# Kernel tuning notes

Hardware: AMD Instinct MI355X
Metric: run time of the kernel (lower is better)

The kernel has to match this reference:

```python
import jax, jax.numpy as jnp
import numpy as np

N_NODES = 100000
N_EDGES = 500000
D = 128          # node embedding dim; in_channels = 2*D = 256
HID = 256
OUT = 1


def setup_inputs() -> dict:
    key = jax.random.key(0)
    k1, k2, k3, k4, k5 = jax.random.split(key, 5)
    z = jax.random.normal(k1, (N_NODES, D), dtype=jnp.float32)
    z2 = jax.random.normal(k2, (N_NODES, D), dtype=jnp.float32)
    edge = jax.random.randint(k3, (2, N_EDGES), 0, N_NODES, dtype=jnp.int64)
    # MLP params (Linear stored as [in, out] for x @ W + b)
    W1 = jax.random.normal(k4, (2 * D, HID), dtype=jnp.float32) * (1.0 / np.sqrt(2 * D))
    b1 = jnp.zeros((HID,), dtype=jnp.float32)
    W2 = jax.random.normal(k5, (HID, OUT), dtype=jnp.float32) * (1.0 / np.sqrt(HID))
    b2 = jnp.zeros((OUT,), dtype=jnp.float32)
    return {"z": z, "z2": z2, "edge": edge, "W1": W1, "b1": b1, "W2": W2, "b2": b2}


def reference(z, z2, edge, W1, b1, W2, b2):
    # Gather node embeddings at edge endpoints, elementwise multiply, concat.
    src, dst = edge[0], edge[1]
    x = jnp.concatenate([z[src] * z[dst], z2[src] * z2[dst]], axis=1)  # [E, 2D]
    # Two-layer MLP (dropout is identity in eval mode), relu, final sigmoid.
    h = jax.nn.relu(x @ W1 + b1)        # [E, HID]
    out = jax.nn.sigmoid(h @ W2 + b2)   # [E, 1]
    return out
```

## Files before the change

### kernel.cpp

```cpp
#include <hip/hip_runtime.h>
#include <hip/hip_bf16.h>
#include <math.h>

typedef _Float16 half8 __attribute__((ext_vector_type(8)));
typedef float f32x4 __attribute__((ext_vector_type(4)));

#define NE 500000
#define ND 128
#define NNODES 100000
#define NT ((NE + 63) / 64)
#define TPB 8

__global__ void prep_w1t_kernel(const float* __restrict__ W1,
                                _Float16* __restrict__ W1T) {
    int i = blockIdx.x * blockDim.x + threadIdx.x;
    int n = i >> 8, k = i & 255;
    W1T[n * 256 + k] = (_Float16)W1[k * 256 + n];
}

__global__ __launch_bounds__(256) void prep_zh_kernel(
    const float* __restrict__ z, const float* __restrict__ z2,
    _Float16* __restrict__ zh, _Float16* __restrict__ z2h) {
    long t = (long)blockIdx.x * 256 + threadIdx.x;
    const float* src; _Float16* dst; long off;
    const long halfn = (long)NNODES * ND / 8;
    if (t < halfn) { src = z;  dst = zh;  off = t * 8; }
    else           { src = z2; dst = z2h; off = (t - halfn) * 8; }
    float4 a = *reinterpret_cast<const float4*>(src + off);
    float4 b = *reinterpret_cast<const float4*>(src + off + 4);
    half8 v;
    v[0] = (_Float16)a.x; v[1] = (_Float16)a.y;
    v[2] = (_Float16)a.z; v[3] = (_Float16)a.w;
    v[4] = (_Float16)b.x; v[5] = (_Float16)b.y;
    v[6] = (_Float16)b.z; v[7] = (_Float16)b.w;
    *reinterpret_cast<half8*>(dst + off) = v;
}

#define PUBLISH_BARRIER() do { \
    asm volatile("s_waitcnt lgkmcnt(0)" ::: "memory"); \
    __builtin_amdgcn_s_barrier(); } while (0)

__global__ __launch_bounds__(512, 1) void edge_mlp_pipe(
    const _Float16* __restrict__ zh, const _Float16* __restrict__ z2h,
    const int* __restrict__ edge,
    const _Float16* __restrict__ w1t,
    const float* __restrict__ b1, const float* __restrict__ W2,
    const float* __restrict__ b2, float* __restrict__ out)
{
    __shared__ _Float16 xs[64 * 256];
    __shared__ float partials[4][64];

    const int tid = threadIdx.x;
    const int lane = tid & 63;
    const int wv = tid >> 6;
    const int mi = wv >> 2;
    const int ni = wv & 3;
    const int l15 = lane & 15;
    const int l4 = lane >> 4;
    const int l5 = lane >> 5;
    const int hz = (lane >> 4) & 1;
    const int c8 = lane & 15;
    const _Float16* gbase = hz ? z2h : zh;

    half8 breg[4][8];
#pragma unroll
    for (int nf = 0; nf < 4; ++nf)
#pragma unroll
        for (int ks = 0; ks < 8; ++ks)
            breg[nf][ks] = *reinterpret_cast<const half8*>(
                w1t + (long)(ni * 64 + nf * 16 + l15) * 256 + ks * 32 + l4 * 8);

    float b1v[4], w2v[4];
#pragma unroll
    for (int nf = 0; nf < 4; ++nf) {
        int col = ni * 64 + nf * 16 + l15;
        b1v[nf] = b1[col];
        w2v[nf] = W2[col];
    }
    const float bias2 = b2[0];

    const int t0 = blockIdx.x * TPB;
    const int tend = (t0 + TPB < NT) ? (t0 + TPB) : NT;

    half8 vs[4], vd[4];
    int idx_nxt;

    {
        long e = (long)t0 * 64 + wv * 8 + (lane & 7); if (e >= NE) e = NE - 1;
        int myidx = edge[((lane >> 3) & 1) ? (NE + e) : e];
#pragma unroll
        for (int i = 0; i < 4; ++i) {
            int el_loc = i * 2 + l5;
            long s = __shfl(myidx, el_loc, 64);
            long d = __shfl(myidx, 8 + el_loc, 64);
            vs[i] = *reinterpret_cast<const half8*>(gbase + s * ND + (c8 << 3));
            vd[i] = *reinterpret_cast<const half8*>(gbase + d * ND + (c8 << 3));
        }
        int t1 = (t0 + 1 < NT) ? t0 + 1 : NT - 1;
        long e1 = (long)t1 * 64 + wv * 8 + (lane & 7); if (e1 >= NE) e1 = NE - 1;
        idx_nxt = edge[((lane >> 3) & 1) ? (NE + e1) : e1];
    }

    for (int t = t0; t < tend; ++t) {
#pragma unroll
        for (int i = 0; i < 4; ++i) {
            int el = wv * 8 + i * 2 + l5;
            half8 p = vs[i] * vd[i];
            int col0 = (hz << 7) + (c8 << 3);
            *reinterpret_cast<half8*>(&xs[el * 256 + (col0 ^ ((el & 7) << 3))]) = p;
        }

        if (t + 1 < tend) {
#pragma unroll
            for (int i = 0; i < 4; ++i) {
                int el_loc = i * 2 + l5;
                long s = __shfl(idx_nxt, el_loc, 64);
                long d = __shfl(idx_nxt, 8 + el_loc, 64);
                vs[i] = *reinterpret_cast<const half8*>(gbase + s * ND + (c8 << 3));
                vd[i] = *reinterpret_cast<const half8*>(gbase + d * ND + (c8 << 3));
            }
            int t2 = (t + 2 < NT) ? t + 2 : NT - 1;
            long e2 = (long)t2 * 64 + wv * 8 + (lane & 7); if (e2 >= NE) e2 = NE - 1;
            idx_nxt = edge[((lane >> 3) & 1) ? (NE + e2) : e2];
        }

        PUBLISH_BARRIER();

        f32x4 acc[2][4];
#pragma unroll
        for (int mf = 0; mf < 2; ++mf)
#pragma unroll
            for (int nf = 0; nf < 4; ++nf)
                acc[mf][nf] = (f32x4){0.f, 0.f, 0.f, 0.f};

#pragma unroll
        for (int ks = 0; ks < 8; ++ks) {
            const int k0 = ks * 32 + l4 * 8;
            half8 a[2];
#pragma unroll
            for (int mf = 0; mf < 2; ++mf) {
                int row = mi * 32 + mf * 16 + l15;
                a[mf] = *reinterpret_cast<const half8*>(
                    &xs[row * 256 + (k0 ^ ((row & 7) << 3))]);
            }
#pragma unroll
            for (int mf = 0; mf < 2; ++mf)
#pragma unroll
                for (int nf = 0; nf < 4; ++nf)
                    acc[mf][nf] = __builtin_amdgcn_mfma_f32_16x16x32_f16(
                        a[mf], breg[nf][ks], acc[mf][nf], 0, 0, 0);
        }

#pragma unroll
        for (int mf = 0; mf < 2; ++mf) {
            float s0 = 0.f, s1 = 0.f, s2 = 0.f, s3 = 0.f;
#pragma unroll
            for (int nf = 0; nf < 4; ++nf) {
                float h0 = fmaxf(acc[mf][nf][0] + b1v[nf], 0.f);
                float h1 = fmaxf(acc[mf][nf][1] + b1v[nf], 0.f);
                float h2 = fmaxf(acc[mf][nf][2] + b1v[nf], 0.f);
                float h3 = fmaxf(acc[mf][nf][3] + b1v[nf], 0.f);
                s0 += h0 * w2v[nf]; s1 += h1 * w2v[nf];
                s2 += h2 * w2v[nf]; s3 += h3 * w2v[nf];
            }
#pragma unroll
            for (int mask = 1; mask < 16; mask <<= 1) {
                s0 += __shfl_xor(s0, mask, 64);
                s1 += __shfl_xor(s1, mask, 64);
                s2 += __shfl_xor(s2, mask, 64);
                s3 += __shfl_xor(s3, mask, 64);
            }
            if (l15 == 0) {
                int rb = mi * 32 + mf * 16 + l4 * 4;
                partials[ni][rb + 0] = s0;
                partials[ni][rb + 1] = s1;
                partials[ni][rb + 2] = s2;
                partials[ni][rb + 3] = s3;
            }
        }
        PUBLISH_BARRIER();

        if (tid < 64) {
            float p = partials[0][tid] + partials[1][tid]
                    + partials[2][tid] + partials[3][tid] + bias2;
            long e = (long)t * 64 + tid;
            if (e < NE) out[e] = 1.0f / (1.0f + expf(-p));
        }
    }
}

__global__ __launch_bounds__(256) void edge_mlp_f32(
    const float* __restrict__ z, const float* __restrict__ z2,
    const int* __restrict__ edge,
    const _Float16* __restrict__ w1t,
    const float* __restrict__ b1, const float* __restrict__ W2,
    const float* __restrict__ b2, float* __restrict__ out)
{
    __shared__ _Float16 xs[64 * 256];
    __shared__ float partials[4][64];
    const int tid = threadIdx.x, lane = tid & 63, wv = tid >> 6;
    const int l15 = lane & 15, l4 = lane >> 4;
    const long eb0 = (long)blockIdx.x * 64;
    {
        const int hz = lane >> 5, c4 = lane & 31;
        const float* base = hz ? z2 : z;
        for (int i = 0; i < 16; ++i) {
            int el = (wv << 4) + i;
            long ee = eb0 + el; if (ee >= NE) ee = NE - 1;
            long s = edge[ee], d = edge[NE + ee];
            float4 a = *reinterpret_cast<const float4*>(base + s * ND + (c4 << 2));
            float4 b = *reinterpret_cast<const float4*>(base + d * ND + (c4 << 2));
            _Float16 p[4] = {(_Float16)(a.x * b.x), (_Float16)(a.y * b.y),
                             (_Float16)(a.z * b.z), (_Float16)(a.w * b.w)};
            int col0 = (hz << 7) + (c4 << 2);
            int o = el * 256 + (col0 ^ ((el & 7) << 3));
            xs[o] = p[0]; xs[o + 1] = p[1]; xs[o + 2] = p[2]; xs[o + 3] = p[3];
        }
    }
    __syncthreads();
    f32x4 acc[4][4];
    for (int m = 0; m < 4; ++m) for (int n = 0; n < 4; ++n) acc[m][n] = (f32x4){0,0,0,0};
    const int ncol0 = wv * 64 + l15;
    for (int ks = 0; ks < 8; ++ks) {
        const int k0 = ks * 32 + l4 * 8;
        half8 a[4], b[4];
        for (int m = 0; m < 4; ++m) {
            int row = m * 16 + l15;
            a[m] = *reinterpret_cast<const half8*>(&xs[row * 256 + (k0 ^ ((row & 7) << 3))]);
        }
        for (int n = 0; n < 4; ++n)
            b[n] = *reinterpret_cast<const half8*>(w1t + (long)(ncol0 + n * 16) * 256 + k0);
        for (int m = 0; m < 4; ++m) for (int n = 0; n < 4; ++n)
            acc[m][n] = __builtin_amdgcn_mfma_f32_16x16x32_f16(a[m], b[n], acc[m][n], 0, 0, 0);
    }
    float b1v[4], w2v[4];
    for (int n = 0; n < 4; ++n) {
        int col = wv * 64 + n * 16 + l15;
        b1v[n] = b1[col]; w2v[n] = W2[col];
    }
    for (int m = 0; m < 4; ++m) {
        float s0 = 0, s1 = 0, s2 = 0, s3 = 0;
        for (int n = 0; n < 4; ++n) {
            float h0 = fmaxf(acc[m][n][0] + b1v[n], 0.f), h1 = fmaxf(acc[m][n][1] + b1v[n], 0.f);
            float h2 = fmaxf(acc[m][n][2] + b1v[n], 0.f), h3 = fmaxf(acc[m][n][3] + b1v[n], 0.f);
            s0 += h0 * w2v[n]; s1 += h1 * w2v[n]; s2 += h2 * w2v[n]; s3 += h3 * w2v[n];
        }
        for (int mask = 1; mask < 16; mask <<= 1) {
            s0 += __shfl_xor(s0, mask, 64); s1 += __shfl_xor(s1, mask, 64);
            s2 += __shfl_xor(s2, mask, 64); s3 += __shfl_xor(s3, mask, 64);
        }
        if (l15 == 0) {
            int rb = m * 16 + l4 * 4;
            partials[wv][rb] = s0; partials[wv][rb + 1] = s1;
            partials[wv][rb + 2] = s2; partials[wv][rb + 3] = s3;
        }
    }
    __syncthreads();
    if (tid < 64) {
        float p = partials[0][tid] + partials[1][tid] + partials[2][tid]
                + partials[3][tid] + b2[0];
        long e = eb0 + tid;
        if (e < NE) out[e] = 1.0f / (1.0f + expf(-p));
    }
}

extern "C" void kernel_launch(void* const* d_in, const int* in_sizes, int n_in,
                              void* d_out, int out_size, void* d_ws, size_t ws_size,
                              hipStream_t stream)
{
    const float* z  = (const float*)d_in[0];
    const float* z2 = (const float*)d_in[1];
    const int*  edge = (const int*)d_in[2];
    const float* W1 = (const float*)d_in[3];
    const float* b1 = (const float*)d_in[4];
    const float* W2 = (const float*)d_in[5];
    const float* b2 = (const float*)d_in[6];
    float* out = (float*)d_out;

    const size_t zh_bytes = (size_t)NNODES * ND * 2;
    const size_t need = 2 * zh_bytes + 256 * 256 * 2;
    const bool mirrors = (ws_size >= need);

    _Float16* zh  = (_Float16*)d_ws;
    _Float16* z2h = (_Float16*)((char*)d_ws + zh_bytes);
    _Float16* w1t = mirrors
        ? (_Float16*)((char*)d_ws + 2 * zh_bytes)
        : (_Float16*)d_ws;

    prep_w1t_kernel<<<256, 256, 0, stream>>>(W1, w1t);
    if (mirrors) {
        prep_zh_kernel<<<12500, 256, 0, stream>>>(z, z2, zh, z2h);
        const int nblk = (NT + TPB - 1) / TPB;
        edge_mlp_pipe<<<nblk, 512, 0, stream>>>(
            zh, z2h, edge, w1t, b1, W2, b2, out);
    } else {
        edge_mlp_f32<<<NT, 256, 0, stream>>>(
            z, z2, edge, w1t, b1, W2, b2, out);
    }
}
```

Measured before the change: 154.4 us.

## Gather endpoint rows into double-buffered LDS via async global_load_lds

Replaces the register-staged gather (load to VGPRs, multiply, store to LDS) with direct global-to-LDS async loads of raw source and destination rows into double-buffered shared arrays. The elementwise product moves into the MFMA operand load, and the output write is spread across all waves. The aim is to drop the VGPR round-trip and overlap the next tile's gather with the current GEMM using a vmcnt-based wait. It doubles the LDS footprint and relies on the swizzle and vmcnt(10) count being right, and the product is now recomputed for each of the two mf fragments.

```diff
diff --git a/kernel.cpp b/kernel.cpp
--- a/kernel.cpp
+++ b/kernel.cpp
@@ -36,18 +36,15 @@
     *reinterpret_cast<half8*>(dst + off) = v;
 }
 
-#define PUBLISH_BARRIER() do { \
-    asm volatile("s_waitcnt lgkmcnt(0)" ::: "memory"); \
-    __builtin_amdgcn_s_barrier(); } while (0)
-
-__global__ __launch_bounds__(512, 1) void edge_mlp_pipe(
+__global__ __launch_bounds__(512, 1) void edge_mlp_dma(
     const _Float16* __restrict__ zh, const _Float16* __restrict__ z2h,
     const int* __restrict__ edge,
     const _Float16* __restrict__ w1t,
     const float* __restrict__ b1, const float* __restrict__ W2,
     const float* __restrict__ b2, float* __restrict__ out)
 {
-    __shared__ _Float16 xs[64 * 256];
+    __shared__ _Float16 rawS[2][64][256];
+    __shared__ _Float16 rawD[2][64][256];
     __shared__ float partials[4][64];
 
     const int tid = threadIdx.x;
@@ -57,10 +54,45 @@
     const int ni = wv & 3;
     const int l15 = lane & 15;
     const int l4 = lane >> 4;
-    const int l5 = lane >> 5;
-    const int hz = (lane >> 4) & 1;
-    const int c8 = lane & 15;
-    const _Float16* gbase = hz ? z2h : zh;
+
+    const int dl5 = lane >> 5;
+    const int dcc = lane & 15;
+    const int dten = (lane >> 4) & 1;
+    const _Float16* dbase = dten ? z2h : zh;
+
+    const int t0 = blockIdx.x * TPB;
+    const int tend = (t0 + TPB < NT) ? (t0 + TPB) : NT;
+
+#define LOAD_IDX(TT, DST) do {                                               \
+        int tt_ = (TT) < (NT - 1) ? (TT) : (NT - 1);                         \
+        long e_ = (long)tt_ * 64 + wv * 8 + (lane & 7);                      \
+        if (e_ >= NE) e_ = NE - 1;                                           \
+        (DST) = edge[(((lane >> 3) & 1) ? (long)NE : 0L) + e_];              \
+    } while (0)
+
+#define ISSUE_DMA(IDXREG, BB) do {                                           \
+        _Pragma("unroll")                                                    \
+        for (int j = 0; j < 4; ++j) {                                        \
+            int sl_ = 2 * j + dl5;                                           \
+            int si_ = __shfl((IDXREG), sl_, 64);                             \
+            int di_ = __shfl((IDXREG), 8 + sl_, 64);                         \
+            int swz_ = (dcc ^ sl_) << 3;  \
+            const _Float16* gs_ = dbase + (long)si_ * ND + swz_;             \
+            const _Float16* gd_ = dbase + (long)di_ * ND + swz_;             \
+            __builtin_amdgcn_global_load_lds(                                \
+                (const void*)gs_, (void*)&rawS[BB][wv * 8 + 2 * j][0], 16, 0, 0); \
+            __builtin_amdgcn_global_load_lds(                                \
+                (const void*)gd_, (void*)&rawD[BB][wv * 8 + 2 * j][0], 16, 0, 0); \
+        }                                                                    \
+    } while (0)
+
+    int idx_cur, idx_new;
+    {
+        int idx0;
+        LOAD_IDX(t0, idx0);
+        ISSUE_DMA(idx0, 0);
+        LOAD_IDX(t0 + 1, idx_cur);
+    }
 
     half8 breg[4][8];
 #pragma unroll
@@ -79,52 +111,15 @@
     }
     const float bias2 = b2[0];
 
-    const int t0 = blockIdx.x * TPB;
-    const int tend = (t0 + TPB < NT) ? (t0 + TPB) : NT;
-
-    half8 vs[4], vd[4];
-    int idx_nxt;
-
-    {
-        long e = (long)t0 * 64 + wv * 8 + (lane & 7); if (e >= NE) e = NE - 1;
-        int myidx = edge[((lane >> 3) & 1) ? (NE + e) : e];
-#pragma unroll
-        for (int i = 0; i < 4; ++i) {
-            int el_loc = i * 2 + l5;
-            long s = __shfl(myidx, el_loc, 64);
-            long d = __shfl(myidx, 8 + el_loc, 64);
-            vs[i] = *reinterpret_cast<const half8*>(gbase + s * ND + (c8 << 3));
-            vd[i] = *reinterpret_cast<const half8*>(gbase + d * ND + (c8 << 3));
-        }
-        int t1 = (t0 + 1 < NT) ? t0 + 1 : NT - 1;
-        long e1 = (long)t1 * 64 + wv * 8 + (lane & 7); if (e1 >= NE) e1 = NE - 1;
-        idx_nxt = edge[((lane >> 3) & 1) ? (NE + e1) : e1];
-    }
-
     for (int t = t0; t < tend; ++t) {
-#pragma unroll
-        for (int i = 0; i < 4; ++i) {
-            int el = wv * 8 + i * 2 + l5;
-            half8 p = vs[i] * vd[i];
-            int col0 = (hz << 7) + (c8 << 3);
-            *reinterpret_cast<half8*>(&xs[el * 256 + (col0 ^ ((el & 7) << 3))]) = p;
-        }
-
-        if (t + 1 < tend) {
-#pragma unroll
-            for (int i = 0; i < 4; ++i) {
-                int el_loc = i * 2 + l5;
-                long s = __shfl(idx_nxt, el_loc, 64);
-                long d = __shfl(idx_nxt, 8 + el_loc, 64);
-                vs[i] = *reinterpret_cast<const half8*>(gbase + s * ND + (c8 << 3));
-                vd[i] = *reinterpret_cast<const half8*>(gbase + d * ND + (c8 << 3));
-            }
-            int t2 = (t + 2 < NT) ? t + 2 : NT - 1;
-            long e2 = (long)t2 * 64 + wv * 8 + (lane & 7); if (e2 >= NE) e2 = NE - 1;
-            idx_nxt = edge[((lane >> 3) & 1) ? (NE + e2) : e2];
-        }
-
-        PUBLISH_BARRIER();
+        const int cur = (t - t0) & 1, nxt = cur ^ 1;
+
+        ISSUE_DMA(idx_cur, nxt);
+        LOAD_IDX(t + 2, idx_new);
+
+        asm volatile("s_waitcnt vmcnt(10)" ::: "memory");
+        __builtin_amdgcn_s_barrier();
+        __builtin_amdgcn_sched_barrier(0);
 
         f32x4 acc[2][4];
 #pragma unroll
@@ -133,22 +128,25 @@
             for (int nf = 0; nf < 4; ++nf)
                 acc[mf][nf] = (f32x4){0.f, 0.f, 0.f, 0.f};
 
+        const _Float16* rs = &rawS[cur][0][0];
+        const _Float16* rd = &rawD[cur][0][0];
 #pragma unroll
         for (int ks = 0; ks < 8; ++ks) {
-            const int k0 = ks * 32 + l4 * 8;
-            half8 a[2];
+            const int c = ks * 4 + l4;
+            const int slot = ((c & 15) ^ (l15 & 7)) | (c & 16);
+            const int so = slot * 8;
 #pragma unroll
             for (int mf = 0; mf < 2; ++mf) {
                 int row = mi * 32 + mf * 16 + l15;
-                a[mf] = *reinterpret_cast<const half8*>(
-                    &xs[row * 256 + (k0 ^ ((row & 7) << 3))]);
-            }
-#pragma unroll
-            for (int mf = 0; mf < 2; ++mf)
+                int o = row * 256 + so;
+                half8 aS = *reinterpret_cast<const half8*>(rs + o);
+                half8 aD = *reinterpret_cast<const half8*>(rd + o);
+                half8 a = aS * aD;
 #pragma unroll
                 for (int nf = 0; nf < 4; ++nf)
                     acc[mf][nf] = __builtin_amdgcn_mfma_f32_16x16x32_f16(
-                        a[mf], breg[nf][ks], acc[mf][nf], 0, 0, 0);
+                        a, breg[nf][ks], acc[mf][nf], 0, 0, 0);
+            }
         }
 
 #pragma unroll
@@ -178,15 +176,21 @@
                 partials[ni][rb + 3] = s3;
             }
         }
-        PUBLISH_BARRIER();
-
-        if (tid < 64) {
-            float p = partials[0][tid] + partials[1][tid]
-                    + partials[2][tid] + partials[3][tid] + bias2;
-            long e = (long)t * 64 + tid;
+        asm volatile("s_waitcnt lgkmcnt(0)" ::: "memory");
+        __builtin_amdgcn_s_barrier();
+        __builtin_amdgcn_sched_barrier(0);
+
+        if (lane < 8) {
+            int r = wv * 8 + lane;
+            float p = partials[0][r] + partials[1][r]
+                    + partials[2][r] + partials[3][r] + bias2;
+            long e = (long)t * 64 + r;
             if (e < NE) out[e] = 1.0f / (1.0f + expf(-p));
         }
-    }
+        idx_cur = idx_new;
+    }
+#undef LOAD_IDX
+#undef ISSUE_DMA
 }
 
 __global__ __launch_bounds__(256) void edge_mlp_f32(
@@ -291,7 +295,7 @@
     if (mirrors) {
         prep_zh_kernel<<<12500, 256, 0, stream>>>(z, z2, zh, z2h);
         const int nblk = (NT + TPB - 1) / TPB;
-        edge_mlp_pipe<<<nblk, 512, 0, stream>>>(
+        edge_mlp_dma<<<nblk, 512, 0, stream>>>(
             zh, z2h, edge, w1t, b1, W2, b2, out);
     } else {
         edge_mlp_f32<<<NT, 256, 0, stream>>>(
```

New measurement: 178.9 us. +15.9%, slower.

## Interleave z/z2 fp16 mirror rows and stage W1 in LDS via async copy

Applied to the files above, without the earlier changes.

Packs z and z2 into one interleaved fp16 row per node so each edge endpoint becomes a single contiguous 512-byte gather, using readlane broadcast indices with half4 per-lane loads. W1 is pre-swizzled and copied into LDS with global_load_lds instead of being held as 32 half8 registers per lane, freeing VGPRs at the cost of 128KB LDS and extra LDS reads per MFMA step. Adds extra barriers per tile and reuses the xs buffer for partial sums. The output writes are spread across waves.

```diff
diff --git a/kernel.cpp b/kernel.cpp
--- a/kernel.cpp
+++ b/kernel.cpp
@@ -2,6 +2,7 @@
 #include <hip/hip_bf16.h>
 #include <math.h>
 
+typedef _Float16 half4 __attribute__((ext_vector_type(4)));
 typedef _Float16 half8 __attribute__((ext_vector_type(8)));
 typedef float f32x4 __attribute__((ext_vector_type(4)));
 
@@ -11,44 +12,48 @@
 #define NT ((NE + 63) / 64)
 #define TPB 8
 
-__global__ void prep_w1t_kernel(const float* __restrict__ W1,
-                                _Float16* __restrict__ W1T) {
-    int i = blockIdx.x * blockDim.x + threadIdx.x;
-    int n = i >> 8, k = i & 255;
-    W1T[n * 256 + k] = (_Float16)W1[k * 256 + n];
-}
-
-__global__ __launch_bounds__(256) void prep_zh_kernel(
+__global__ __launch_bounds__(256) void prep_zi_kernel(
     const float* __restrict__ z, const float* __restrict__ z2,
-    _Float16* __restrict__ zh, _Float16* __restrict__ z2h) {
+    _Float16* __restrict__ zi) {
     long t = (long)blockIdx.x * 256 + threadIdx.x;
-    const float* src; _Float16* dst; long off;
-    const long halfn = (long)NNODES * ND / 8;
-    if (t < halfn) { src = z;  dst = zh;  off = t * 8; }
-    else           { src = z2; dst = z2h; off = (t - halfn) * 8; }
-    float4 a = *reinterpret_cast<const float4*>(src + off);
-    float4 b = *reinterpret_cast<const float4*>(src + off + 4);
+    long idx = t * 8;
+    if (idx >= (long)NNODES * 256) return;
+    int node = (int)(idx >> 8), col = (int)(idx & 255);
+    const float* src = (col < 128) ? (z + (long)node * 128 + col)
+                                   : (z2 + (long)node * 128 + (col - 128));
+    float4 a = *reinterpret_cast<const float4*>(src);
+    float4 b = *reinterpret_cast<const float4*>(src + 4);
     half8 v;
     v[0] = (_Float16)a.x; v[1] = (_Float16)a.y;
     v[2] = (_Float16)a.z; v[3] = (_Float16)a.w;
     v[4] = (_Float16)b.x; v[5] = (_Float16)b.y;
     v[6] = (_Float16)b.z; v[7] = (_Float16)b.w;
-    *reinterpret_cast<half8*>(dst + off) = v;
+    *reinterpret_cast<half8*>(zi + idx) = v;
+}
+
+__global__ void prep_w1s_kernel(const float* __restrict__ W1,
+                                _Float16* __restrict__ w1s) {
+    int i = blockIdx.x * blockDim.x + threadIdx.x;
+    int col = i >> 8, k = i & 255;
+    int kk = (((k >> 3) ^ (col & 7)) << 3) | (k & 7);
+    w1s[col * 256 + kk] = (_Float16)W1[(long)k * 256 + col];
 }
 
 #define PUBLISH_BARRIER() do { \
     asm volatile("s_waitcnt lgkmcnt(0)" ::: "memory"); \
-    __builtin_amdgcn_s_barrier(); } while (0)
-
-__global__ __launch_bounds__(512, 1) void edge_mlp_pipe(
-    const _Float16* __restrict__ zh, const _Float16* __restrict__ z2h,
+    __builtin_amdgcn_s_barrier(); \
+    __builtin_amdgcn_sched_barrier(0); } while (0)
+
+__global__ __launch_bounds__(512, 1) void edge_mlp_v8(
+    const _Float16* __restrict__ zi,
     const int* __restrict__ edge,
-    const _Float16* __restrict__ w1t,
+    const _Float16* __restrict__ w1s,
     const float* __restrict__ b1, const float* __restrict__ W2,
     const float* __restrict__ b2, float* __restrict__ out)
 {
+    __shared__ _Float16 w1lds[256 * 256];
     __shared__ _Float16 xs[64 * 256];
-    __shared__ float partials[4][64];
+    float* ps = (float*)xs;
 
     const int tid = threadIdx.x;
     const int lane = tid & 63;
@@ -57,18 +62,15 @@
     const int ni = wv & 3;
     const int l15 = lane & 15;
     const int l4 = lane >> 4;
-    const int l5 = lane >> 5;
-    const int hz = (lane >> 4) & 1;
-    const int c8 = lane & 15;
-    const _Float16* gbase = hz ? z2h : zh;
-
-    half8 breg[4][8];
-#pragma unroll
-    for (int nf = 0; nf < 4; ++nf)
-#pragma unroll
-        for (int ks = 0; ks < 8; ++ks)
-            breg[nf][ks] = *reinterpret_cast<const half8*>(
-                w1t + (long)(ni * 64 + nf * 16 + l15) * 256 + ks * 32 + l4 * 8);
+
+    {
+        const char* gsrc = (const char*)w1s + (long)(wv * 16) * 1024 + lane * 16;
+        char* ldst = (char*)w1lds + (wv * 16) * 1024;
+#pragma unroll
+        for (int i = 0; i < 16; ++i)
+            __builtin_amdgcn_global_load_lds(
+                (const void*)(gsrc + i * 1024), (void*)(ldst + i * 1024), 16, 0, 0);
+    }
 
     float b1v[4], w2v[4];
 #pragma unroll
@@ -82,48 +84,42 @@
     const int t0 = blockIdx.x * TPB;
     const int tend = (t0 + TPB < NT) ? (t0 + TPB) : NT;
 
-    half8 vs[4], vd[4];
-    int idx_nxt;
-
-    {
-        long e = (long)t0 * 64 + wv * 8 + (lane & 7); if (e >= NE) e = NE - 1;
-        int myidx = edge[((lane >> 3) & 1) ? (NE + e) : e];
-#pragma unroll
-        for (int i = 0; i < 4; ++i) {
-            int el_loc = i * 2 + l5;
-            long s = __shfl(myidx, el_loc, 64);
-            long d = __shfl(myidx, 8 + el_loc, 64);
-            vs[i] = *reinterpret_cast<const half8*>(gbase + s * ND + (c8 << 3));
-            vd[i] = *reinterpret_cast<const half8*>(gbase + d * ND + (c8 << 3));
-        }
-        int t1 = (t0 + 1 < NT) ? t0 + 1 : NT - 1;
-        long e1 = (long)t1 * 64 + wv * 8 + (lane & 7); if (e1 >= NE) e1 = NE - 1;
-        idx_nxt = edge[((lane >> 3) & 1) ? (NE + e1) : e1];
-    }
+    half4 vs[8], vd[8];
+    int idx_cur, idx_nxt;
+
+#define LOAD_IDX(TT, DST) do {                                               \
+        long tt_ = (TT); if (tt_ > NT - 1) tt_ = NT - 1;                     \
+        long e_ = tt_ * 64 + wv * 8 + (lane & 7);                            \
+        if (e_ >= NE) e_ = NE - 1;                                           \
+        (DST) = edge[(((lane >> 3) & 1) ? (long)NE : 0L) + e_];              \
+    } while (0)
+
+#define ISSUE_GATHER(IDXREG) do {                                            \
+        _Pragma("unroll")                                                    \
+        for (int j = 0; j < 8; ++j) {                                        \
+            int s_ = __builtin_amdgcn_readlane((IDXREG), j);                 \
+            int d_ = __builtin_amdgcn_readlane((IDXREG), 8 + j);             \
+            vs[j] = *reinterpret_cast<const half4*>(zi + (long)s_ * 256 + lane * 4); \
+            vd[j] = *reinterpret_cast<const half4*>(zi + (long)d_ * 256 + lane * 4); \
+        }                                                                    \
+    } while (0)
+
+    LOAD_IDX(t0, idx_cur);
+    ISSUE_GATHER(idx_cur);
+    LOAD_IDX(t0 + 1, idx_cur);
 
     for (int t = t0; t < tend; ++t) {
 #pragma unroll
-        for (int i = 0; i < 4; ++i) {
-            int el = wv * 8 + i * 2 + l5;
-            half8 p = vs[i] * vd[i];
-            int col0 = (hz << 7) + (c8 << 3);
-            *reinterpret_cast<half8*>(&xs[el * 256 + (col0 ^ ((el & 7) << 3))]) = p;
-        }
-
+        for (int j = 0; j < 8; ++j) {
+            int e = wv * 8 + j;
+            half4 p = vs[j] * vd[j];
+            int boff = e * 512 + ((lane * 8) ^ ((e & 7) << 4));
+            *reinterpret_cast<half4*>((char*)xs + boff) = p;
+        }
         if (t + 1 < tend) {
-#pragma unroll
-            for (int i = 0; i < 4; ++i) {
-                int el_loc = i * 2 + l5;
-                long s = __shfl(idx_nxt, el_loc, 64);
-                long d = __shfl(idx_nxt, 8 + el_loc, 64);
-                vs[i] = *reinterpret_cast<const half8*>(gbase + s * ND + (c8 << 3));
-                vd[i] = *reinterpret_cast<const half8*>(gbase + d * ND + (c8 << 3));
-            }
-            int t2 = (t + 2 < NT) ? t + 2 : NT - 1;
-            long e2 = (long)t2 * 64 + wv * 8 + (lane & 7); if (e2 >= NE) e2 = NE - 1;
-            idx_nxt = edge[((lane >> 3) & 1) ? (NE + e2) : e2];
-        }
-
+            ISSUE_GATHER(idx_cur);
+            LOAD_IDX(t + 2, idx_nxt);
+        }
         PUBLISH_BARRIER();
 
         f32x4 acc[2][4];
@@ -135,21 +131,28 @@
 
 #pragma unroll
         for (int ks = 0; ks < 8; ++ks) {
-            const int k0 = ks * 32 + l4 * 8;
-            half8 a[2];
+            const int kb = ks * 64 + l4 * 16;
+            half8 a[2], bfr[4];
 #pragma unroll
             for (int mf = 0; mf < 2; ++mf) {
-                int row = mi * 32 + mf * 16 + l15;
+                int r = mi * 32 + mf * 16 + l15;
                 a[mf] = *reinterpret_cast<const half8*>(
-                    &xs[row * 256 + (k0 ^ ((row & 7) << 3))]);
+                    (const char*)xs + r * 512 + (kb ^ ((r & 7) << 4)));
+            }
+#pragma unroll
+            for (int nf = 0; nf < 4; ++nf) {
+                int c = ni * 64 + nf * 16 + l15;
+                bfr[nf] = *reinterpret_cast<const half8*>(
+                    (const char*)w1lds + c * 512 + (kb ^ ((c & 7) << 4)));
             }
 #pragma unroll
             for (int mf = 0; mf < 2; ++mf)
 #pragma unroll
                 for (int nf = 0; nf < 4; ++nf)
                     acc[mf][nf] = __builtin_amdgcn_mfma_f32_16x16x32_f16(
-                        a[mf], breg[nf][ks], acc[mf][nf], 0, 0, 0);
-        }
+                        a[mf], bfr[nf], acc[mf][nf], 0, 0, 0);
+        }
+        PUBLISH_BARRIER();
 
 #pragma unroll
         for (int mf = 0; mf < 2; ++mf) {
@@ -172,27 +175,31 @@
             }
             if (l15 == 0) {
                 int rb = mi * 32 + mf * 16 + l4 * 4;
-                partials[ni][rb + 0] = s0;
-                partials[ni][rb + 1] = s1;
-                partials[ni][rb + 2] = s2;
-                partials[ni][rb + 3] = s3;
+                ps[ni * 64 + rb + 0] = s0;
+                ps[ni * 64 + rb + 1] = s1;
+                ps[ni * 64 + rb + 2] = s2;
+                ps[ni * 64 + rb + 3] = s3;
             }
         }
         PUBLISH_BARRIER();
 
-        if (tid < 64) {
-            float p = partials[0][tid] + partials[1][tid]
-                    + partials[2][tid] + partials[3][tid] + bias2;
-            long e = (long)t * 64 + tid;
+        if (lane < 8) {
+            int r = wv * 8 + lane;
+            float p = ps[r] + ps[64 + r] + ps[128 + r] + ps[192 + r] + bias2;
+            long e = (long)t * 64 + r;
             if (e < NE) out[e] = 1.0f / (1.0f + expf(-p));
         }
-    }
+        idx_cur = idx_nxt;
+        PUBLISH_BARRIER();
+    }
+#undef LOAD_IDX
+#undef ISSUE_GATHER
 }
 
 __global__ __launch_bounds__(256) void edge_mlp_f32(
     const float* __restrict__ z, const float* __restrict__ z2,
     const int* __restrict__ edge,
-    const _Float16* __restrict__ w1t,
+    const _Float16* __restrict__ w1s,
     const float* __restrict__ b1, const float* __restrict__ W2,
     const float* __restrict__ b2, float* __restrict__ out)
 {
@@ -210,26 +217,27 @@
             long s = edge[ee], d = edge[NE + ee];
             float4 a = *reinterpret_cast<const float4*>(base + s * ND + (c4 << 2));
             float4 b = *reinterpret_cast<const float4*>(base + d * ND + (c4 << 2));
-            _Float16 p[4] = {(_Float16)(a.x * b.x), (_Float16)(a.y * b.y),
-                             (_Float16)(a.z * b.z), (_Float16)(a.w * b.w)};
             int col0 = (hz << 7) + (c4 << 2);
-            int o = el * 256 + (col0 ^ ((el & 7) << 3));
-            xs[o] = p[0]; xs[o + 1] = p[1]; xs[o + 2] = p[2]; xs[o + 3] = p[3];
+            int boff = el * 512 + (((col0 * 2) & ~15) ^ ((el & 7) << 4)) + ((col0 * 2) & 15);
+            _Float16* q = (_Float16*)((char*)xs + boff);
+            q[0] = (_Float16)(a.x * b.x); q[1] = (_Float16)(a.y * b.y);
+            q[2] = (_Float16)(a.z * b.z); q[3] = (_Float16)(a.w * b.w);
         }
     }
     __syncthreads();
     f32x4 acc[4][4];
     for (int m = 0; m < 4; ++m) for (int n = 0; n < 4; ++n) acc[m][n] = (f32x4){0,0,0,0};
-    const int ncol0 = wv * 64 + l15;
     for (int ks = 0; ks < 8; ++ks) {
-        const int k0 = ks * 32 + l4 * 8;
+        const int kb = ks * 64 + l4 * 16;
         half8 a[4], b[4];
         for (int m = 0; m < 4; ++m) {
-            int row = m * 16 + l15;
-            a[m] = *reinterpret_cast<const half8*>(&xs[row * 256 + (k0 ^ ((row & 7) << 3))]);
-        }
-        for (int n = 0; n < 4; ++n)
-            b[n] = *reinterpret_cast<const half8*>(w1t + (long)(ncol0 + n * 16) * 256 + k0);
+            int r = m * 16 + l15;
+            a[m] = *reinterpret_cast<const half8*>((const char*)xs + r * 512 + (kb ^ ((r & 7) << 4)));
+        }
+        for (int n = 0; n < 4; ++n) {
+            int c = wv * 64 + n * 16 + l15;
+            b[n] = *reinterpret_cast<const half8*>((const char*)w1s + c * 512 + (kb ^ ((c & 7) << 4)));
+        }
         for (int m = 0; m < 4; ++m) for (int n = 0; n < 4; ++n)
             acc[m][n] = __builtin_amdgcn_mfma_f32_16x16x32_f16(a[m], b[n], acc[m][n], 0, 0, 0);
     }
@@ -277,24 +285,22 @@
     const float* b2 = (const float*)d_in[6];
     float* out = (float*)d_out;
 
-    const size_t zh_bytes = (size_t)NNODES * ND * 2;
-    const size_t need = 2 * zh_bytes + 256 * 256 * 2;
-    const bool mirrors = (ws_size >= need);
-
-    _Float16* zh  = (_Float16*)d_ws;
-    _Float16* z2h = (_Float16*)((char*)d_ws + zh_bytes);
-    _Float16* w1t = mirrors
-        ? (_Float16*)((char*)d_ws + 2 * zh_bytes)
-        : (_Float16*)d_ws;
-
-    prep_w1t_kernel<<<256, 256, 0, stream>>>(W1, w1t);
+    const size_t zi_bytes = (size_t)NNODES * 256 * 2;
+    const size_t w1_bytes = 256 * 256 * 2;
+    const bool mirrors = (ws_size >= zi_bytes + w1_bytes);
+
+    _Float16* zi  = (_Float16*)d_ws;
+    _Float16* w1s = mirrors ? (_Float16*)((char*)d_ws + zi_bytes)
+                            : (_Float16*)d_ws;
+
+    prep_w1s_kernel<<<256, 256, 0, stream>>>(W1, w1s);
     if (mirrors) {
-        prep_zh_kernel<<<12500, 256, 0, stream>>>(z, z2, zh, z2h);
+        prep_zi_kernel<<<12500, 256, 0, stream>>>(z, z2, zi);
         const int nblk = (NT + TPB - 1) / TPB;
-        edge_mlp_pipe<<<nblk, 512, 0, stream>>>(
-            zh, z2h, edge, w1t, b1, W2, b2, out);
+        edge_mlp_v8<<<nblk, 512, 0, stream>>>(
+            zi, edge, w1s, b1, W2, b2, out);
     } else {
         edge_mlp_f32<<<NT, 256, 0, stream>>>(
-            z, z2, edge, w1t, b1, W2, b2, out);
-    }
-}
+            z, z2, edge, w1s, b1, W2, b2, out);
+    }
+}
```

Result: slower. 162.3 us (+5.2%).
